# Kernel tuning notes

Hardware: AMD Instinct MI355X
Metric: run time of the kernel (lower is better)

## Reference

```python
import jax, jax.numpy as jnp
import numpy as np

B, C, T, F = 256, 1, 8192, 16


def _lrelu(h):
    return jnp.where(h > 0, h, 0.01 * h)


def _adain(h, style):
    # h: (B, T, 8), style: (B, 8, 2)
    scale = style[:, None, :, 0]          # (B, 1, 8)
    bias = style[:, None, :, 1]           # (B, 1, 8)
    mu = jnp.mean(h, axis=-1, keepdims=True)
    sigma = jnp.std(h, axis=-1, ddof=1, keepdims=True) + 1e-6  # torch.std is unbiased
    return scale * (h - mu) / sigma + bias


def setup_inputs() -> dict:
    key = jax.random.key(0)
    ks = jax.random.split(key, 20)
    g = lambda k, shp, s=0.2: (jax.random.normal(k, shp, dtype=jnp.float32) * s)
    inp = {
        "x": jax.random.normal(ks[0], (B, C, T), dtype=jnp.float32),
        "metadata": jax.random.normal(ks[1], (B, F), dtype=jnp.float32),
        # MetadataMLP: F->64->128->64 (total_channels*2 = 32*2)
        "mw1": g(ks[2], (F, 64)), "mb1": g(ks[3], (64,)),
        "mw2": g(ks[4], (64, 128)), "mb2": g(ks[5], (128,)),
        "mw3": g(ks[6], (128, 64)), "mb3": g(ks[7], (64,)),
        # main chain 1->8->8->8->8->1
        "w1": g(ks[8], (1, 8)), "b1": g(ks[9], (8,)),
        "w2": g(ks[10], (8, 8)), "b2": g(ks[11], (8,)),
        "w3": g(ks[12], (8, 8)), "b3": g(ks[13], (8,)),
        "w4": g(ks[14], (8, 8)), "b4": g(ks[15], (8,)),
        "w5": g(ks[16], (8, 1)), "b5": g(ks[17], (1,)),
    }
    return inp


def reference(x, metadata, mw1, mb1, mw2, mb2, mw3, mb3,
              w1, b1, w2, b2, w3, b3, w4, b4, w5, b5):
    # style MLP
    s = jax.nn.relu(metadata @ mw1 + mb1)
    s = jax.nn.relu(s @ mw2 + mb2)
    s = s @ mw3 + mb3                     # (B, 64)
    s1, s2, s3, s4 = jnp.split(s, 4, axis=1)  # each (B, 16)
    s1, s2, s3, s4 = (t.reshape(-1, 8, 2) for t in (s1, s2, s3, s4))

    h = jnp.transpose(x, (0, 2, 1))       # (B, T, 1)
    h = h @ w1 + b1                       # (B, T, 8)
    h = _lrelu(_adain(h, s1))
    h = h @ w2 + b2
    h = _lrelu(_adain(h, s2))
    h = h @ w3 + b3
    h = _lrelu(_adain(h, s3))
    h = h @ w4 + b4
    h = _lrelu(_adain(h, s4))
    h = h @ w5 + b5                       # (B, T, 1)
    out = _lrelu(h)
    return jnp.transpose(out, (0, 2, 1))  # (B, 1, T)
```

## Files before the change

kernel.cpp:

```cpp
#include <hip/hip_runtime.h>

#define BATCH   256
#define TLEN    8192
#define TPB     256
#define EPT     4
#define CHUNKS  (TLEN / (TPB * EPT))
#define PSTRIDE 320


__device__ __forceinline__ float rowmean8(const float* __restrict__ p) {
    return (((p[0] + p[1]) + (p[2] + p[3])) + ((p[4] + p[5]) + (p[6] + p[7]))) * 0.125f;
}

__device__ __forceinline__ float lrelu(float t) { return fmaxf(t, 0.01f * t); }

__global__ __launch_bounds__(128) void prep_kernel(
    const float* __restrict__ metadata,
    const float* __restrict__ mw1, const float* __restrict__ mb1,
    const float* __restrict__ mw2, const float* __restrict__ mb2,
    const float* __restrict__ mw3, const float* __restrict__ mb3,
    const float* __restrict__ w1, const float* __restrict__ b1,
    const float* __restrict__ w2, const float* __restrict__ b2,
    const float* __restrict__ w3, const float* __restrict__ b3,
    const float* __restrict__ w4, const float* __restrict__ b4,
    const float* __restrict__ w5, const float* __restrict__ b5,
    float* __restrict__ P)
{
    const int b   = blockIdx.x;
    const int tid = threadIdx.x;
    __shared__ float md[16];
    __shared__ float h1[64];
    __shared__ float h2[128];
    __shared__ float s[64];
    __shared__ float la[8], lc[8], sc1[8];

    if (tid < 16) md[tid] = metadata[b * 16 + tid];
    __syncthreads();

    if (tid < 64) {
        float a = mb1[tid];
        #pragma unroll
        for (int k = 0; k < 16; ++k) a = fmaf(md[k], mw1[k * 64 + tid], a);
        h1[tid] = fmaxf(a, 0.f);
    }
    __syncthreads();

    {
        float a = mb2[tid];
        #pragma unroll 16
        for (int k = 0; k < 64; ++k) a = fmaf(h1[k], mw2[k * 128 + tid], a);
        h2[tid] = fmaxf(a, 0.f);
    }
    __syncthreads();

    if (tid < 64) {
        float a = mb3[tid];
        #pragma unroll 16
        for (int k = 0; k < 128; ++k) a = fmaf(h2[k], mw3[k * 64 + tid], a);
        s[tid] = a;
    }
    if (tid < 8) {
        la[tid]  = w1[tid] - rowmean8(w1);
        lc[tid]  = b1[tid] - rowmean8(b1);
    }
    __syncthreads();
    if (tid < 8) sc1[tid] = s[2 * tid];
    __syncthreads();

    float* __restrict__ p = P + b * PSTRIDE;

    if (tid == 0) {
        float A = 0.f, B = 0.f, C = 0.f;
        #pragma unroll
        for (int j = 0; j < 8; ++j) {
            A = fmaf(la[j], la[j], A);
            B = fmaf(la[j], lc[j], B);
            C = fmaf(lc[j], lc[j], C);
        }
        p[24] = A; p[25] = 2.f * B; p[26] = C; p[27] = b5[0];
    }
    if (tid < 8) {
        p[tid]      = la[tid] * sc1[tid];
        p[8 + tid]  = lc[tid] * sc1[tid];
        p[16 + tid] = s[2 * tid + 1];
        p[32 + 64 + tid]       = b2[tid] - rowmean8(b2);
        p[32 + 72 + tid]       = s[16 + 2 * tid];
        p[32 + 80 + tid]       = s[16 + 2 * tid + 1];
        p[120 + 64 + tid]      = b3[tid] - rowmean8(b3);
        p[120 + 72 + tid]      = s[32 + 2 * tid];
        p[120 + 80 + tid]      = s[32 + 2 * tid + 1];
        p[208 + 64 + tid]      = b4[tid] - rowmean8(b4);
        p[208 + 72 + tid]      = s[48 + 2 * tid];
        p[208 + 80 + tid]      = s[48 + 2 * tid + 1];
        p[296 + tid]           = w5[tid];
    }
    if (tid >= 64) {
        int i = tid - 64;
        p[32 + i]  = w2[i] - rowmean8(w2 + (i & 56));
        p[120 + i] = w3[i] - rowmean8(w3 + (i & 56));
        p[208 + i] = w4[i] - rowmean8(w4 + (i & 56));
    }
}

__global__ __launch_bounds__(TPB, 4) void adain_main_kernel(
    const float* __restrict__ x, const float* __restrict__ P, float* __restrict__ out)
{
    __shared__ float4 pbuf[76];
    float* __restrict__ p = (float*)pbuf;

    const int tid   = threadIdx.x;
    const int b     = blockIdx.x / CHUNKS;
    const int chunk = blockIdx.x % CHUNKS;

    if (tid < 76) pbuf[tid] = ((const float4*)(P + b * PSTRIDE))[tid];
    __syncthreads();

    const float cA = p[24], cB2 = p[25], cC = p[26], lb5 = p[27];

    const float4* __restrict__ x4   = (const float4*)x;
    float4* __restrict__       out4 = (float4*)out;
    const int i4 = b * (TLEN / 4) + chunk * TPB + tid;

    const float4 v = x4[i4];
    const float ve[4] = {v.x, v.y, v.z, v.w};
    float h[4][8];

    #pragma unroll
    for (int e = 0; e < 4; ++e) {
        float var = fmaxf(fmaf(ve[e], fmaf(ve[e], cA, cB2), cC), 0.f);
        float inv = __builtin_amdgcn_rcpf(
                        __builtin_amdgcn_sqrtf(var * (1.f / 7.f)) + 1e-6f);
        #pragma unroll
        for (int j = 0; j < 8; ++j) {
            float d = fmaf(ve[e], p[j], p[8 + j]);
            h[e][j] = lrelu(fmaf(d, inv, p[16 + j]));
        }
    }

    #pragma unroll
    for (int l = 0; l < 3; ++l) {
        const float* __restrict__ wc = p + 32 + l * 88;
        const float* __restrict__ cb = wc + 64;
        const float* __restrict__ sc = wc + 72;
        const float* __restrict__ sb = wc + 80;

        float g[4][8];
        #pragma unroll
        for (int e = 0; e < 4; ++e)
            #pragma unroll
            for (int j = 0; j < 8; ++j) g[e][j] = cb[j];

        #pragma unroll
        for (int k = 0; k < 8; ++k) {
            const float4 wa = *(const float4*)(wc + k * 8);
            const float4 wb = *(const float4*)(wc + k * 8 + 4);
            const float wr[8] = {wa.x, wa.y, wa.z, wa.w, wb.x, wb.y, wb.z, wb.w};
            #pragma unroll
            for (int e = 0; e < 4; ++e) {
                const float hk = h[e][k];
                #pragma unroll
                for (int j = 0; j < 8; ++j) g[e][j] = fmaf(hk, wr[j], g[e][j]);
            }
        }

        #pragma unroll
        for (int e = 0; e < 4; ++e) {
            float var = 0.f;
            #pragma unroll
            for (int j = 0; j < 8; ++j) var = fmaf(g[e][j], g[e][j], var);
            float inv = __builtin_amdgcn_rcpf(
                            __builtin_amdgcn_sqrtf(var * (1.f / 7.f)) + 1e-6f);
            #pragma unroll
            for (int j = 0; j < 8; ++j)
                h[e][j] = lrelu(fmaf(g[e][j] * inv, sc[j], sb[j]));
        }
    }

    float oe[4];
    #pragma unroll
    for (int e = 0; e < 4; ++e) {
        float a = lb5;
        #pragma unroll
        for (int k = 0; k < 8; ++k) a = fmaf(h[e][k], p[296 + k], a);
        oe[e] = lrelu(a);
    }
    out4[i4] = make_float4(oe[0], oe[1], oe[2], oe[3]);
}

extern "C" void kernel_launch(void* const* d_in, const int* in_sizes, int n_in,
                              void* d_out, int out_size, void* d_ws, size_t ws_size,
                              hipStream_t stream)
{
    const float* x        = (const float*)d_in[0];
    const float* metadata = (const float*)d_in[1];
    const float* mw1      = (const float*)d_in[2];
    const float* mb1      = (const float*)d_in[3];
    const float* mw2      = (const float*)d_in[4];
    const float* mb2      = (const float*)d_in[5];
    const float* mw3      = (const float*)d_in[6];
    const float* mb3      = (const float*)d_in[7];
    const float* w1       = (const float*)d_in[8];
    const float* b1       = (const float*)d_in[9];
    const float* w2       = (const float*)d_in[10];
    const float* b2       = (const float*)d_in[11];
    const float* w3       = (const float*)d_in[12];
    const float* b3       = (const float*)d_in[13];
    const float* w4       = (const float*)d_in[14];
    const float* b4       = (const float*)d_in[15];
    const float* w5       = (const float*)d_in[16];
    const float* b5       = (const float*)d_in[17];

    float* P = (float*)d_ws;

    prep_kernel<<<BATCH, 128, 0, stream>>>(
        metadata, mw1, mb1, mw2, mb2, mw3, mb3,
        w1, b1, w2, b2, w3, b3, w4, b4, w5, b5, P);
    adain_main_kernel<<<BATCH * CHUNKS, TPB, 0, stream>>>(x, P, (float*)d_out);
}
```

Measured before the change: 113.2 us.

## Read params via scalar loads, halve elements per thread, fold sqrt7 into scales

The main kernel no longer stages per-batch parameters in shared memory or syncs. It reads them directly from global memory, which are uniform and therefore candidates for scalar loads. Each thread now handles 2 elements instead of 4, launch bounds allow 6 blocks per CU, and the 1/7 variance factor is folded into the precomputed scale and epsilon. This aims to cut LDS traffic, barriers and per-element multiplies and to raise occupancy, at the cost of more blocks and narrower vector memory accesses.

```diff
diff --git a/kernel.cpp b/kernel.cpp
--- a/kernel.cpp
+++ b/kernel.cpp
@@ -3,9 +3,11 @@
 #define BATCH   256
 #define TLEN    8192
 #define TPB     256
-#define EPT     4
+#define EPT     2
 #define CHUNKS  (TLEN / (TPB * EPT))
 #define PSTRIDE 320
+#define SQRT7   2.6457513110645906f
+#define C1      2.6457513110645906e-6f
 
 
 __device__ __forceinline__ float rowmean8(const float* __restrict__ p) {
@@ -32,7 +34,7 @@
     __shared__ float h1[64];
     __shared__ float h2[128];
     __shared__ float s[64];
-    __shared__ float la[8], lc[8], sc1[8];
+    __shared__ float la[8], lc[8];
 
     if (tid < 16) md[tid] = metadata[b * 16 + tid];
     __syncthreads();
@@ -59,12 +61,11 @@
         for (int k = 0; k < 128; ++k) a = fmaf(h2[k], mw3[k * 64 + tid], a);
         s[tid] = a;
     }
-    if (tid < 8) {
-        la[tid]  = w1[tid] - rowmean8(w1);
-        lc[tid]  = b1[tid] - rowmean8(b1);
-    }
-    __syncthreads();
-    if (tid < 8) sc1[tid] = s[2 * tid];
+    if (tid >= 64 && tid < 72) {
+        int j = tid - 64;
+        la[j] = w1[j] - rowmean8(w1);
+        lc[j] = b1[j] - rowmean8(b1);
+    }
     __syncthreads();
 
     float* __restrict__ p = P + b * PSTRIDE;
@@ -80,19 +81,20 @@
         p[24] = A; p[25] = 2.f * B; p[26] = C; p[27] = b5[0];
     }
     if (tid < 8) {
-        p[tid]      = la[tid] * sc1[tid];
-        p[8 + tid]  = lc[tid] * sc1[tid];
+        const float sc1 = s[2 * tid] * SQRT7;
+        p[tid]      = la[tid] * sc1;
+        p[8 + tid]  = lc[tid] * sc1;
         p[16 + tid] = s[2 * tid + 1];
-        p[32 + 64 + tid]       = b2[tid] - rowmean8(b2);
-        p[32 + 72 + tid]       = s[16 + 2 * tid];
-        p[32 + 80 + tid]       = s[16 + 2 * tid + 1];
-        p[120 + 64 + tid]      = b3[tid] - rowmean8(b3);
-        p[120 + 72 + tid]      = s[32 + 2 * tid];
-        p[120 + 80 + tid]      = s[32 + 2 * tid + 1];
-        p[208 + 64 + tid]      = b4[tid] - rowmean8(b4);
-        p[208 + 72 + tid]      = s[48 + 2 * tid];
-        p[208 + 80 + tid]      = s[48 + 2 * tid + 1];
-        p[296 + tid]           = w5[tid];
+        p[32 + 64 + tid]  = b2[tid] - rowmean8(b2);
+        p[32 + 72 + tid]  = s[16 + 2 * tid] * SQRT7;
+        p[32 + 80 + tid]  = s[16 + 2 * tid + 1];
+        p[120 + 64 + tid] = b3[tid] - rowmean8(b3);
+        p[120 + 72 + tid] = s[32 + 2 * tid] * SQRT7;
+        p[120 + 80 + tid] = s[32 + 2 * tid + 1];
+        p[208 + 64 + tid] = b4[tid] - rowmean8(b4);
+        p[208 + 72 + tid] = s[48 + 2 * tid] * SQRT7;
+        p[208 + 80 + tid] = s[48 + 2 * tid + 1];
+        p[296 + tid]      = w5[tid];
     }
     if (tid >= 64) {
         int i = tid - 64;
@@ -102,89 +104,77 @@
     }
 }
 
-__global__ __launch_bounds__(TPB, 4) void adain_main_kernel(
+__global__ __launch_bounds__(TPB, 6) void adain_main_kernel(
     const float* __restrict__ x, const float* __restrict__ P, float* __restrict__ out)
 {
-    __shared__ float4 pbuf[76];
-    float* __restrict__ p = (float*)pbuf;
-
     const int tid   = threadIdx.x;
     const int b     = blockIdx.x / CHUNKS;
     const int chunk = blockIdx.x % CHUNKS;
 
-    if (tid < 76) pbuf[tid] = ((const float4*)(P + b * PSTRIDE))[tid];
-    __syncthreads();
+    const float* __restrict__ p = P + b * PSTRIDE;
 
     const float cA = p[24], cB2 = p[25], cC = p[26], lb5 = p[27];
 
-    const float4* __restrict__ x4   = (const float4*)x;
-    float4* __restrict__       out4 = (float4*)out;
-    const int i4 = b * (TLEN / 4) + chunk * TPB + tid;
-
-    const float4 v = x4[i4];
-    const float ve[4] = {v.x, v.y, v.z, v.w};
-    float h[4][8];
+    const int i2 = b * (TLEN / 2) + chunk * TPB + tid;
+    const float2 v2 = ((const float2*)x)[i2];
+    const float ve[2] = {v2.x, v2.y};
+    float h[2][8];
 
     #pragma unroll
-    for (int e = 0; e < 4; ++e) {
-        float var = fmaxf(fmaf(ve[e], fmaf(ve[e], cA, cB2), cC), 0.f);
-        float inv = __builtin_amdgcn_rcpf(
-                        __builtin_amdgcn_sqrtf(var * (1.f / 7.f)) + 1e-6f);
+    for (int e = 0; e < 2; ++e) {
+        const float var = fmaxf(fmaf(ve[e], fmaf(ve[e], cA, cB2), cC), 0.f);
+        const float r   = __builtin_amdgcn_rcpf(__builtin_amdgcn_sqrtf(var) + C1);
         #pragma unroll
         for (int j = 0; j < 8; ++j) {
-            float d = fmaf(ve[e], p[j], p[8 + j]);
-            h[e][j] = lrelu(fmaf(d, inv, p[16 + j]));
+            const float d = fmaf(ve[e], p[j], p[8 + j]);
+            h[e][j] = lrelu(fmaf(d, r, p[16 + j]));
         }
     }
 
     #pragma unroll
     for (int l = 0; l < 3; ++l) {
-        const float* __restrict__ wc = p + 32 + l * 88;
-        const float* __restrict__ cb = wc + 64;
-        const float* __restrict__ sc = wc + 72;
-        const float* __restrict__ sb = wc + 80;
-
-        float g[4][8];
-        #pragma unroll
-        for (int e = 0; e < 4; ++e)
-            #pragma unroll
-            for (int j = 0; j < 8; ++j) g[e][j] = cb[j];
-
-        #pragma unroll
-        for (int k = 0; k < 8; ++k) {
-            const float4 wa = *(const float4*)(wc + k * 8);
-            const float4 wb = *(const float4*)(wc + k * 8 + 4);
-            const float wr[8] = {wa.x, wa.y, wa.z, wa.w, wb.x, wb.y, wb.z, wb.w};
-            #pragma unroll
-            for (int e = 0; e < 4; ++e) {
-                const float hk = h[e][k];
+        const float* __restrict__ w = p + 32 + l * 88;
+
+        float cbv[8], sbv[8];
+        #pragma unroll
+        for (int j = 0; j < 8; ++j) { cbv[j] = w[64 + j]; sbv[j] = w[80 + j]; }
+
+        float g[2][8];
+        #pragma unroll
+        for (int e = 0; e < 2; ++e)
+            #pragma unroll
+            for (int j = 0; j < 8; ++j)
+                g[e][j] = fmaf(h[e][0], w[j], cbv[j]);
+
+        #pragma unroll
+        for (int k = 1; k < 8; ++k)
+            #pragma unroll
+            for (int e = 0; e < 2; ++e)
                 #pragma unroll
-                for (int j = 0; j < 8; ++j) g[e][j] = fmaf(hk, wr[j], g[e][j]);
-            }
+                for (int j = 0; j < 8; ++j)
+                    g[e][j] = fmaf(h[e][k], w[k * 8 + j], g[e][j]);
+
+        #pragma unroll
+        for (int e = 0; e < 2; ++e) {
+            float var = 0.f;
+            #pragma unroll
+            for (int j = 0; j < 8; ++j) var = fmaf(g[e][j], g[e][j], var);
+            const float r = __builtin_amdgcn_rcpf(__builtin_amdgcn_sqrtf(var) + C1);
+            #pragma unroll
+            for (int j = 0; j < 8; ++j)
+                h[e][j] = lrelu(fmaf(g[e][j] * r, w[72 + j], sbv[j]));
         }
-
-        #pragma unroll
-        for (int e = 0; e < 4; ++e) {
-            float var = 0.f;
-            #pragma unroll
-            for (int j = 0; j < 8; ++j) var = fmaf(g[e][j], g[e][j], var);
-            float inv = __builtin_amdgcn_rcpf(
-                            __builtin_amdgcn_sqrtf(var * (1.f / 7.f)) + 1e-6f);
-            #pragma unroll
-            for (int j = 0; j < 8; ++j)
-                h[e][j] = lrelu(fmaf(g[e][j] * inv, sc[j], sb[j]));
-        }
-    }
-
-    float oe[4];
+    }
+
+    float oe[2];
     #pragma unroll
-    for (int e = 0; e < 4; ++e) {
+    for (int e = 0; e < 2; ++e) {
         float a = lb5;
         #pragma unroll
         for (int k = 0; k < 8; ++k) a = fmaf(h[e][k], p[296 + k], a);
         oe[e] = lrelu(a);
     }
-    out4[i4] = make_float4(oe[0], oe[1], oe[2], oe[3]);
+    ((float2*)out)[i2] = make_float2(oe[0], oe[1]);
 }
 
 extern "C" void kernel_launch(void* const* d_in, const int* in_sizes, int n_in,
```

Result: slower. 118.2 us (+4.4%).
